# Optimization experiments

Measured on AMD Instinct MI355X. Metric: run time of the kernel, lower is better.

Reference implementation:

```python
import jax, jax.numpy as jnp
import numpy as np

DIM = 512
HEADS = 8
HEAD_DIM = DIM // HEADS
SCALING = float(np.sqrt(HEAD_DIM))
B, S = 8, 2048


def setup_inputs() -> dict:
    key = jax.random.key(0)
    ks = jax.random.split(key, 6)
    x = jax.random.normal(ks[0], (B, S, DIM), dtype=jnp.float32)
    mask = jax.random.randint(ks[1], (B, S), 0, 2).astype(bool)
    mask = mask.at[:, 0].set(False)  # guarantee at least one unmasked key per row
    lim_qkv = 1.0 / np.sqrt(DIM)
    Wqkv = jax.random.uniform(ks[2], (3 * DIM, DIM), minval=-lim_qkv, maxval=lim_qkv, dtype=jnp.float32)
    bqkv = jax.random.uniform(ks[3], (3 * DIM,), minval=-lim_qkv, maxval=lim_qkv, dtype=jnp.float32)
    Wout = jax.random.uniform(ks[4], (DIM, DIM), minval=-lim_qkv, maxval=lim_qkv, dtype=jnp.float32)
    bout = jax.random.uniform(ks[5], (DIM,), minval=-lim_qkv, maxval=lim_qkv, dtype=jnp.float32)
    ln_g = jnp.ones((DIM,), dtype=jnp.float32)
    ln_b = jnp.zeros((DIM,), dtype=jnp.float32)
    return {"x": x, "mask": mask, "Wqkv": Wqkv, "bqkv": bqkv, "Wout": Wout, "bout": bout, "ln_g": ln_g, "ln_b": ln_b}


def reference(x, mask, Wqkv, bqkv, Wout, bout, ln_g, ln_b):
    b, s, _ = x.shape
    qkv = x @ Wqkv.T + bqkv                                   # [b, s, 3*dim]
    qkv = qkv.reshape(b, s, HEADS, HEAD_DIM, 3)               # torch reshape semantics (interleaved)
    q = qkv[..., 0]                                           # [b, s, h, d]
    k = qkv[..., 1]
    v = jax.nn.elu(qkv[..., 2])
    attn = jnp.einsum('bqhd,bkhd->bhqk', q, k) / SCALING      # [b, h, s, s]
    bias = jnp.where(mask[:, None, None, :], -jnp.inf, 0.0).astype(attn.dtype)
    attn = jax.nn.softmax(attn + bias, axis=-1)
    out = jnp.einsum('bhqk,bkhd->bqhd', attn, v).reshape(b, s, DIM)
    out = out @ Wout.T + bout
    mu = jnp.mean(out, axis=-1, keepdims=True)
    var = jnp.var(out, axis=-1, keepdims=True)
    out = (out - mu) / jnp.sqrt(var + 1e-5) * ln_g + ln_b
    return jax.nn.elu(out)
```

## Files before the change

### kernel.cpp

```cpp
#include <hip/hip_runtime.h>

#define DIM 512
#define HEADS 8
#define HD 64
#define NB 8
#define NS 2048
#define SCALE_INV 0.125f
#define NEG_BIG -1e30f
#define QSZ 8388608

typedef __attribute__((ext_vector_type(8))) short bf16x8;
typedef __attribute__((ext_vector_type(4))) float f32x4;

__device__ __forceinline__ float elu_f(float x) {
    return x > 0.0f ? x : (__expf(x) - 1.0f);
}
__device__ __forceinline__ short f2bf(float x) {
    union { float f; unsigned u; } v; v.f = x;
    unsigned r = v.u + 0x7FFFu + ((v.u >> 16) & 1u);
    return (short)(r >> 16);
}
__device__ __forceinline__ unsigned pack_bf_t(float a, float b) {
    union { float f; unsigned u; } va, vb; va.f = a; vb.f = b;
    return (va.u >> 16) | (vb.u & 0xFFFF0000u);
}

#define X4 2097152
#define W14 196608
#define W24 65536
__global__ __launch_bounds__(256) void prep(
    const float* __restrict__ x, const float* __restrict__ Wqkv,
    const float* __restrict__ bqkv, const float* __restrict__ Wout,
    short* __restrict__ xb, short* __restrict__ Wp,
    float* __restrict__ bp, short* __restrict__ Wob)
{
    int i = blockIdx.x * 256 + threadIdx.x;
    if (i < X4) {
        float4 v = *(const float4*)(x + (size_t)i * 4);
        ushort4 o; o.x = (unsigned short)f2bf(v.x); o.y = (unsigned short)f2bf(v.y);
        o.z = (unsigned short)f2bf(v.z); o.w = (unsigned short)f2bf(v.w);
        *(ushort4*)(xb + (size_t)i * 4) = o;
    } else if (i < X4 + W14) {
        int j = i - X4;
        int np = j >> 7, k = (j & 127) * 4;
        int w = np >> 9, h = (np >> 6) & 7, d = np & 63;
        int n = h * 192 + d * 3 + w;
        float4 v = *(const float4*)(Wqkv + (size_t)n * 512 + k);
        ushort4 o; o.x = (unsigned short)f2bf(v.x); o.y = (unsigned short)f2bf(v.y);
        o.z = (unsigned short)f2bf(v.z); o.w = (unsigned short)f2bf(v.w);
        *(ushort4*)(Wp + (size_t)np * 512 + k) = o;
    } else if (i < X4 + W14 + W24) {
        int j = i - X4 - W14;
        float4 v = *(const float4*)(Wout + (size_t)j * 4);
        ushort4 o; o.x = (unsigned short)f2bf(v.x); o.y = (unsigned short)f2bf(v.y);
        o.z = (unsigned short)f2bf(v.z); o.w = (unsigned short)f2bf(v.w);
        *(ushort4*)(Wob + (size_t)j * 4) = o;
    } else {
        int j = i - X4 - W14 - W24;
        int w = j >> 9, h = (j >> 6) & 7, d = j & 63;
        bp[j] = bqkv[h * 192 + d * 3 + w];
    }
}

__global__ __launch_bounds__(256) void qkv_mfma(
    const short* __restrict__ A, const short* __restrict__ Bw,
    const float* __restrict__ bp, short* __restrict__ QKV)
{
    __shared__ short smem[2 * 128 * 64];
    short* As = smem;
    short* Bs = smem + 128 * 64;
    const int t = threadIdx.x, lane = t & 63, wv = t >> 6;
    const int c = lane & 15, quad = lane >> 4;
    const int wr = wv >> 1, wc = wv & 1;
    const int m0 = blockIdx.x * 128, n0 = blockIdx.y * 128;
    f32x4 acc[4][4];
    #pragma unroll
    for (int mi = 0; mi < 4; ++mi)
        #pragma unroll
        for (int nj = 0; nj < 4; ++nj)
            #pragma unroll
            for (int i = 0; i < 4; ++i) acc[mi][nj][i] = 0.0f;

    for (int k0 = 0; k0 < 512; k0 += 64) {
        if (k0) __syncthreads();
        #pragma unroll
        for (int p = 0; p < 4; ++p) {
            int idx = p * 256 + t, r = idx >> 3, cb = idx & 7;
            *(uint4*)&As[r * 64 + ((cb ^ (r & 7)) * 8)] =
                *(const uint4*)(A + (size_t)(m0 + r) * 512 + k0 + cb * 8);
            *(uint4*)&Bs[r * 64 + ((cb ^ (r & 7)) * 8)] =
                *(const uint4*)(Bw + (size_t)(n0 + r) * 512 + k0 + cb * 8);
        }
        __syncthreads();
        bf16x8 af[4][2], bfr[4][2];
        #pragma unroll
        for (int mi = 0; mi < 4; ++mi) {
            int ar = wr * 64 + mi * 16 + c;
            af[mi][0] = *(const bf16x8*)&As[ar * 64 + ((quad       ^ (ar & 7)) * 8)];
            af[mi][1] = *(const bf16x8*)&As[ar * 64 + (((4 + quad) ^ (ar & 7)) * 8)];
        }
        #pragma unroll
        for (int nj = 0; nj < 4; ++nj) {
            int br = wc * 64 + nj * 16 + c;
            bfr[nj][0] = *(const bf16x8*)&Bs[br * 64 + ((quad       ^ (br & 7)) * 8)];
            bfr[nj][1] = *(const bf16x8*)&Bs[br * 64 + (((4 + quad) ^ (br & 7)) * 8)];
        }
        #pragma unroll
        for (int mi = 0; mi < 4; ++mi)
            #pragma unroll
            for (int nj = 0; nj < 4; ++nj) {
                acc[mi][nj] = __builtin_amdgcn_mfma_f32_16x16x32_bf16(af[mi][0], bfr[nj][0], acc[mi][nj], 0, 0, 0);
                acc[mi][nj] = __builtin_amdgcn_mfma_f32_16x16x32_bf16(af[mi][1], bfr[nj][1], acc[mi][nj], 0, 0, 0);
            }
    }

    const int w  = n0 >> 9;
    const int b  = m0 >> 11;
    const int hh = ((n0 + wc * 64) >> 6) & 7;
    float bv[4];
    #pragma unroll
    for (int nj = 0; nj < 4; ++nj) bv[nj] = bp[n0 + wc * 64 + nj * 16 + c];

    if (w < 2) {
        short* out = QKV + (size_t)w * QSZ + (size_t)(b * 8 + hh) * NS * 64;
        #pragma unroll
        for (int mi = 0; mi < 4; ++mi)
            #pragma unroll
            for (int i = 0; i < 4; ++i) {
                int s = (m0 & (NS - 1)) + wr * 64 + mi * 16 + quad * 4 + i;
                #pragma unroll
                for (int nj = 0; nj < 4; ++nj)
                    out[(size_t)s * 64 + nj * 16 + c] = f2bf(acc[mi][nj][i] + bv[nj]);
            }
    } else {
        __syncthreads();
        short* T = smem;
        #pragma unroll
        for (int mi = 0; mi < 4; ++mi)
            #pragma unroll
            for (int i = 0; i < 4; ++i) {
                int ml = wr * 64 + mi * 16 + quad * 4 + i;
                int mb = ml >> 3, mr = ml & 7;
                #pragma unroll
                for (int nj = 0; nj < 4; ++nj) {
                    int nl = wc * 64 + nj * 16 + c;
                    T[nl * 128 + ((mb ^ (nl & 15)) * 8) + mr] =
                        f2bf(elu_f(acc[mi][nj][i] + bv[nj]));
                }
            }
        __syncthreads();
        short* Vt = QKV + (size_t)2 * QSZ;
        #pragma unroll
        for (int p = 0; p < 8; ++p) {
            int idx = p * 256 + t, row = idx >> 4, ch = idx & 15;
            uint4 v = *(const uint4*)&T[row * 128 + ((ch ^ (row & 15)) * 8)];
            int d = row & 63;
            int h2 = ((n0 + row) >> 6) & 7;
            int sg = (m0 & (NS - 1)) + ch * 8;
            int kt = sg >> 6, ks = sg & 63;
            *(uint4*)(Vt + (((size_t)(b * 8 + h2) * 32 + kt) * 64 + d) * 64 + ks) = v;
        }
    }
}

__global__ __launch_bounds__(256, 4) void attn_mfma(
    const short* __restrict__ Qg, const short* __restrict__ Kg,
    const short* __restrict__ Vg, const int* __restrict__ mask,
    short* __restrict__ O)
{
    __shared__ short QP[64 * 64];
    __shared__ short Ks[64 * 64];
    __shared__ short Vs[64 * 64];
    __shared__ float msk[64];

    const int t = threadIdx.x;
    const int lane = t & 63;
    const int wv = t >> 6;
    const int c = lane & 15;
    const int quad = lane >> 4;
    const int bid = blockIdx.x;
    const int qt = bid & 31;
    const int h  = (bid >> 5) & 7;
    const int b  = bid >> 8;
    const int g  = b * 8 + h;
    const size_t base = (size_t)g * NS * HD;
    const int q0 = qt * 64;

    #pragma unroll
    for (int p = 0; p < 2; ++p) {
        int idx = p * 256 + t, r = idx >> 3, cb = idx & 7;
        *(uint4*)&QP[r * 64 + ((cb ^ (r & 7)) * 8)] =
            *(const uint4*)(Qg + base + (size_t)(q0 + r) * HD + cb * 8);
    }
    __syncthreads();

    const int mq = wv * 16 + c;
    const bf16x8 bq0 = *(const bf16x8*)&QP[mq * 64 + ((quad       ^ (mq & 7)) * 8)];
    const bf16x8 bq1 = *(const bf16x8*)&QP[mq * 64 + (((4 + quad) ^ (mq & 7)) * 8)];

    f32x4 o[4];
    #pragma unroll
    for (int dc = 0; dc < 4; ++dc)
        #pragma unroll
        for (int i = 0; i < 4; ++i) o[dc][i] = 0.0f;
    float lp = 0.0f;

    const int prow = wv * 16 + c;
    const int prot = 8 * (c & 7);

    for (int kt = 0; kt < 32; ++kt) {
        const int k0 = kt * 64;
        __syncthreads();
        #pragma unroll
        for (int p = 0; p < 2; ++p) {
            int idx = p * 256 + t, r = idx >> 3, cb = idx & 7;
            *(uint4*)&Ks[r * 64 + ((cb ^ (r & 7)) * 8)] =
                *(const uint4*)(Kg + base + (size_t)(k0 + r) * HD + cb * 8);
            *(uint4*)&Vs[r * 64 + (((cb * 8 + 8 * (r & 7)) & 63))] =
                *(const uint4*)(Vg + (((size_t)g * 32 + kt) * 64 + r) * 64 + cb * 8);
        }
        if (t < 64) msk[t] = mask[b * NS + k0 + t] ? NEG_BIG : 0.0f;
        __syncthreads();

        f32x4 st[4];
        #pragma unroll
        for (int ks = 0; ks < 4; ++ks) {
            int kr = ks * 16 + c;
            bf16x8 ak0 = *(const bf16x8*)&Ks[kr * 64 + ((quad       ^ (kr & 7)) * 8)];
            bf16x8 ak1 = *(const bf16x8*)&Ks[kr * 64 + (((4 + quad) ^ (kr & 7)) * 8)];
            f32x4 a = {0.0f, 0.0f, 0.0f, 0.0f};
            a = __builtin_amdgcn_mfma_f32_16x16x32_bf16(ak0, bq0, a, 0, 0, 0);
            a = __builtin_amdgcn_mfma_f32_16x16x32_bf16(ak1, bq1, a, 0, 0, 0);
            st[ks] = a;
        }

        #pragma unroll
        for (int ks = 0; ks < 4; ++ks) {
            float4 mb = *(const float4*)&msk[ks * 16 + quad * 4];
            float p0 = __expf(st[ks][0] * SCALE_INV + mb.x);
            float p1 = __expf(st[ks][1] * SCALE_INV + mb.y);
            float p2 = __expf(st[ks][2] * SCALE_INV + mb.z);
            float p3 = __expf(st[ks][3] * SCALE_INV + mb.w);
            lp += (p0 + p1) + (p2 + p3);
            uint2 pk;
            pk.x = pack_bf_t(p0, p1);
            pk.y = pack_bf_t(p2, p3);
            *(uint2*)&QP[prow * 64 + ((ks * 16 + quad * 4 + prot) & 63)] = pk;
        }

        bf16x8 bp0 = *(const bf16x8*)&QP[prow * 64 + ((quad * 8 + prot) & 63)];
        bf16x8 bp1 = *(const bf16x8*)&QP[prow * 64 + ((32 + quad * 8 + prot) & 63)];
        #pragma unroll
        for (int dc = 0; dc < 4; ++dc) {
            int d = dc * 16 + c;
            int vrot = 8 * (d & 7);
            bf16x8 av0 = *(const bf16x8*)&Vs[d * 64 + ((quad * 8 + vrot) & 63)];
            bf16x8 av1 = *(const bf16x8*)&Vs[d * 64 + ((32 + quad * 8 + vrot) & 63)];
            o[dc] = __builtin_amdgcn_mfma_f32_16x16x32_bf16(av0, bp0, o[dc], 0, 0, 0);
            o[dc] = __builtin_amdgcn_mfma_f32_16x16x32_bf16(av1, bp1, o[dc], 0, 0, 0);
        }
    }

    lp += __shfl_xor(lp, 16);
    lp += __shfl_xor(lp, 32);
    float inv = 1.0f / lp;

    int q = q0 + wv * 16 + c;
    short* orow = O + ((size_t)(b * NS + q)) * DIM + h * HD + quad * 4;
    #pragma unroll
    for (int dc = 0; dc < 4; ++dc) {
        uint2 pk;
        pk.x = (unsigned)(unsigned short)f2bf(o[dc][0] * inv)
             | ((unsigned)(unsigned short)f2bf(o[dc][1] * inv) << 16);
        pk.y = (unsigned)(unsigned short)f2bf(o[dc][2] * inv)
             | ((unsigned)(unsigned short)f2bf(o[dc][3] * inv) << 16);
        *(uint2*)(orow + dc * 16) = pk;
    }
}

__global__ __launch_bounds__(256) void out_mfma(
    const short* __restrict__ A, const short* __restrict__ Bw,
    const float* __restrict__ bias, float* __restrict__ Z)
{
    __shared__ short smem[2 * 128 * 64];
    short* As = smem;
    short* Bs = smem + 128 * 64;
    const int t = threadIdx.x, lane = t & 63, wv = t >> 6;
    const int c = lane & 15, quad = lane >> 4;
    const int wr = wv >> 1, wc = wv & 1;
    const int m0 = blockIdx.x * 128, n0 = blockIdx.y * 128;
    f32x4 acc[4][4];
    #pragma unroll
    for (int mi = 0; mi < 4; ++mi)
        #pragma unroll
        for (int nj = 0; nj < 4; ++nj)
            #pragma unroll
            for (int i = 0; i < 4; ++i) acc[mi][nj][i] = 0.0f;

    for (int k0 = 0; k0 < 512; k0 += 64) {
        if (k0) __syncthreads();
        #pragma unroll
        for (int p = 0; p < 4; ++p) {
            int idx = p * 256 + t, r = idx >> 3, cb = idx & 7;
            *(uint4*)&As[r * 64 + ((cb ^ (r & 7)) * 8)] =
                *(const uint4*)(A + (size_t)(m0 + r) * 512 + k0 + cb * 8);
            *(uint4*)&Bs[r * 64 + ((cb ^ (r & 7)) * 8)] =
                *(const uint4*)(Bw + (size_t)(n0 + r) * 512 + k0 + cb * 8);
        }
        __syncthreads();
        bf16x8 af[4][2], bfr[4][2];
        #pragma unroll
        for (int mi = 0; mi < 4; ++mi) {
            int ar = wr * 64 + mi * 16 + c;
            af[mi][0] = *(const bf16x8*)&As[ar * 64 + ((quad       ^ (ar & 7)) * 8)];
            af[mi][1] = *(const bf16x8*)&As[ar * 64 + (((4 + quad) ^ (ar & 7)) * 8)];
        }
        #pragma unroll
        for (int nj = 0; nj < 4; ++nj) {
            int br = wc * 64 + nj * 16 + c;
            bfr[nj][0] = *(const bf16x8*)&Bs[br * 64 + ((quad       ^ (br & 7)) * 8)];
            bfr[nj][1] = *(const bf16x8*)&Bs[br * 64 + (((4 + quad) ^ (br & 7)) * 8)];
        }
        #pragma unroll
        for (int mi = 0; mi < 4; ++mi)
            #pragma unroll
            for (int nj = 0; nj < 4; ++nj) {
                acc[mi][nj] = __builtin_amdgcn_mfma_f32_16x16x32_bf16(af[mi][0], bfr[nj][0], acc[mi][nj], 0, 0, 0);
                acc[mi][nj] = __builtin_amdgcn_mfma_f32_16x16x32_bf16(af[mi][1], bfr[nj][1], acc[mi][nj], 0, 0, 0);
            }
    }
    #pragma unroll
    for (int mi = 0; mi < 4; ++mi)
        #pragma unroll
        for (int i = 0; i < 4; ++i) {
            int mrow = m0 + wr * 64 + mi * 16 + quad * 4 + i;
            #pragma unroll
            for (int nj = 0; nj < 4; ++nj) {
                int n = n0 + wc * 64 + nj * 16 + c;
                Z[(size_t)mrow * 512 + n] = acc[mi][nj][i] + bias[n];
            }
        }
}

__global__ __launch_bounds__(256) void ln_elu(
    const float* __restrict__ Z, const float* __restrict__ g,
    const float* __restrict__ bt, float* __restrict__ out)
{
    const int row = blockIdx.x;
    const float* z = Z + (size_t)row * DIM;
    const int t = threadIdx.x;
    float v0 = z[t], v1 = z[t + 256];
    float s  = v0 + v1;
    float ss = v0 * v0 + v1 * v1;
    #pragma unroll
    for (int off = 32; off > 0; off >>= 1) {
        s  += __shfl_down(s, off);
        ss += __shfl_down(ss, off);
    }
    __shared__ float rs[4], rss[4];
    int wid = t >> 6, lane = t & 63;
    if (lane == 0) { rs[wid] = s; rss[wid] = ss; }
    __syncthreads();
    float S1 = rs[0] + rs[1] + rs[2] + rs[3];
    float S2 = rss[0] + rss[1] + rss[2] + rss[3];
    float mu  = S1 * (1.0f / DIM);
    float var = S2 * (1.0f / DIM) - mu * mu;
    float rstd = rsqrtf(var + 1e-5f);
    float y0 = (v0 - mu) * rstd * g[t]       + bt[t];
    float y1 = (v1 - mu) * rstd * g[t + 256] + bt[t + 256];
    out[(size_t)row * DIM + t]       = elu_f(y0);
    out[(size_t)row * DIM + t + 256] = elu_f(y1);
}

extern "C" void kernel_launch(void* const* d_in, const int* in_sizes, int n_in,
                              void* d_out, int out_size, void* d_ws, size_t ws_size,
                              hipStream_t stream)
{
    const float* x    = (const float*)d_in[0];
    const int*   mask = (const int*)d_in[1];
    const float* Wqkv = (const float*)d_in[2];
    const float* bqkv = (const float*)d_in[3];
    const float* Wout = (const float*)d_in[4];
    const float* bout = (const float*)d_in[5];
    const float* ln_g = (const float*)d_in[6];
    const float* ln_b = (const float*)d_in[7];
    float* out = (float*)d_out;

    short* xb   = (short*)d_ws;
    short* Wp   = xb + QSZ;
    short* Wob  = Wp + 786432;
    short* QKV  = Wob + 262144;
    short* ATTb = QKV + 3 * (size_t)QSZ;
    float* bp   = (float*)(ATTb + QSZ);
    float* Zb   = bp + 1536;

    prep<<<9222, 256, 0, stream>>>(x, Wqkv, bqkv, Wout, xb, Wp, bp, Wob);
    qkv_mfma<<<dim3(128, 12), 256, 0, stream>>>(xb, Wp, bp, QKV);
    attn_mfma<<<2048, 256, 0, stream>>>(QKV, QKV + QSZ, QKV + 2 * (size_t)QSZ, mask, ATTb);
    out_mfma<<<dim3(128, 4), 256, 0, stream>>>(ATTb, Wob, bout, Zb);
    ln_elu<<<NB * NS, 256, 0, stream>>>(Zb, ln_g, ln_b, out);
}
```

Before: 271.5 us.

## Double-buffer attention K/V via direct global-to-LDS loads with 128-query blocks

Attention now uses 512-thread blocks covering 128 queries. K, V and mask tiles are double-buffered in shared memory and loaded with global_load_lds, so the next tile's fetch overlaps compute and one barrier per iteration is removed. The QKV and output GEMMs also switch to direct-to-LDS loads, and all three matrix-core loops raise wave priority with s_setprio. The mask-to-float conversion moves into the prep kernel. The cost is more shared memory per block and reliance on the compiler placing the correct waitcnt before each barrier. The mask buffer is also placed in the tail of the Z scratch buffer.

```diff
diff --git a/kernel.cpp b/kernel.cpp
--- a/kernel.cpp
+++ b/kernel.cpp
@@ -25,14 +25,27 @@
     return (va.u >> 16) | (vb.u & 0xFFFF0000u);
 }
 
+__device__ __forceinline__ void gload16(const void* g, void* l) {
+    __builtin_amdgcn_global_load_lds(
+        (const __attribute__((address_space(1))) unsigned*)g,
+        (__attribute__((address_space(3))) unsigned*)l, 16, 0, 0);
+}
+__device__ __forceinline__ void gload4(const void* g, void* l) {
+    __builtin_amdgcn_global_load_lds(
+        (const __attribute__((address_space(1))) unsigned*)g,
+        (__attribute__((address_space(3))) unsigned*)l, 4, 0, 0);
+}
+
 #define X4 2097152
 #define W14 196608
 #define W24 65536
 __global__ __launch_bounds__(256) void prep(
     const float* __restrict__ x, const float* __restrict__ Wqkv,
     const float* __restrict__ bqkv, const float* __restrict__ Wout,
+    const int* __restrict__ mask,
     short* __restrict__ xb, short* __restrict__ Wp,
-    float* __restrict__ bp, short* __restrict__ Wob)
+    float* __restrict__ bp, short* __restrict__ Wob,
+    float* __restrict__ maskf)
 {
     int i = blockIdx.x * 256 + threadIdx.x;
     if (i < X4) {
@@ -55,10 +68,13 @@
         ushort4 o; o.x = (unsigned short)f2bf(v.x); o.y = (unsigned short)f2bf(v.y);
         o.z = (unsigned short)f2bf(v.z); o.w = (unsigned short)f2bf(v.w);
         *(ushort4*)(Wob + (size_t)j * 4) = o;
-    } else {
+    } else if (i < X4 + W14 + W24 + 1536) {
         int j = i - X4 - W14 - W24;
         int w = j >> 9, h = (j >> 6) & 7, d = j & 63;
         bp[j] = bqkv[h * 192 + d * 3 + w];
+    } else {
+        int j = i - X4 - W14 - W24 - 1536;
+        maskf[j] = mask[j] ? NEG_BIG : 0.0f;
     }
 }
 
@@ -72,6 +88,8 @@
     const int t = threadIdx.x, lane = t & 63, wv = t >> 6;
     const int c = lane & 15, quad = lane >> 4;
     const int wr = wv >> 1, wc = wv & 1;
+    const int rsub = lane >> 3;
+    const int csA = (lane & 7) ^ rsub;
     const int m0 = blockIdx.x * 128, n0 = blockIdx.y * 128;
     f32x4 acc[4][4];
     #pragma unroll
@@ -85,11 +103,9 @@
         if (k0) __syncthreads();
         #pragma unroll
         for (int p = 0; p < 4; ++p) {
-            int idx = p * 256 + t, r = idx >> 3, cb = idx & 7;
-            *(uint4*)&As[r * 64 + ((cb ^ (r & 7)) * 8)] =
-                *(const uint4*)(A + (size_t)(m0 + r) * 512 + k0 + cb * 8);
-            *(uint4*)&Bs[r * 64 + ((cb ^ (r & 7)) * 8)] =
-                *(const uint4*)(Bw + (size_t)(n0 + r) * 512 + k0 + cb * 8);
+            int r = p * 32 + wv * 8 + rsub;
+            gload16(A  + (size_t)(m0 + r) * 512 + k0 + csA * 8, &As[(p * 4 + wv) * 512]);
+            gload16(Bw + (size_t)(n0 + r) * 512 + k0 + csA * 8, &Bs[(p * 4 + wv) * 512]);
         }
         __syncthreads();
         bf16x8 af[4][2], bfr[4][2];
@@ -105,6 +121,7 @@
             bfr[nj][0] = *(const bf16x8*)&Bs[br * 64 + ((quad       ^ (br & 7)) * 8)];
             bfr[nj][1] = *(const bf16x8*)&Bs[br * 64 + (((4 + quad) ^ (br & 7)) * 8)];
         }
+        __builtin_amdgcn_s_setprio(1);
         #pragma unroll
         for (int mi = 0; mi < 4; ++mi)
             #pragma unroll
@@ -112,6 +129,7 @@
                 acc[mi][nj] = __builtin_amdgcn_mfma_f32_16x16x32_bf16(af[mi][0], bfr[nj][0], acc[mi][nj], 0, 0, 0);
                 acc[mi][nj] = __builtin_amdgcn_mfma_f32_16x16x32_bf16(af[mi][1], bfr[nj][1], acc[mi][nj], 0, 0, 0);
             }
+        __builtin_amdgcn_s_setprio(0);
     }
 
     const int w  = n0 >> 9;
@@ -163,15 +181,15 @@
     }
 }
 
-__global__ __launch_bounds__(256, 4) void attn_mfma(
+__global__ __launch_bounds__(512, 6) void attn_mfma(
     const short* __restrict__ Qg, const short* __restrict__ Kg,
-    const short* __restrict__ Vg, const int* __restrict__ mask,
+    const short* __restrict__ Vg, const float* __restrict__ maskf,
     short* __restrict__ O)
 {
-    __shared__ short QP[64 * 64];
-    __shared__ short Ks[64 * 64];
-    __shared__ short Vs[64 * 64];
-    __shared__ float msk[64];
+    __shared__ short QP[128 * 64];
+    __shared__ short Ks[2][64 * 64];
+    __shared__ short Vs[2][64 * 64];
+    __shared__ float msk[2][64];
 
     const int t = threadIdx.x;
     const int lane = t & 63;
@@ -179,18 +197,27 @@
     const int c = lane & 15;
     const int quad = lane >> 4;
     const int bid = blockIdx.x;
-    const int qt = bid & 31;
-    const int h  = (bid >> 5) & 7;
-    const int b  = bid >> 8;
+    const int qt = bid & 15;
+    const int h  = (bid >> 4) & 7;
+    const int b  = bid >> 7;
     const int g  = b * 8 + h;
     const size_t base = (size_t)g * NS * HD;
-    const int q0 = qt * 64;
+    const int q0 = qt * 128;
+
+    const int rsub = lane >> 3;
+    const int csA  = (lane & 7) ^ rsub;
+    const int csV  = ((lane & 7) - rsub) & 7;
 
     #pragma unroll
     for (int p = 0; p < 2; ++p) {
-        int idx = p * 256 + t, r = idx >> 3, cb = idx & 7;
-        *(uint4*)&QP[r * 64 + ((cb ^ (r & 7)) * 8)] =
-            *(const uint4*)(Qg + base + (size_t)(q0 + r) * HD + cb * 8);
+        int r = wv * 16 + p * 8 + rsub;
+        gload16(Qg + base + (size_t)(q0 + r) * HD + csA * 8, &QP[(wv * 2 + p) * 512]);
+    }
+    {
+        int r = wv * 8 + rsub;
+        gload16(Kg + base + (size_t)r * HD + csA * 8, &Ks[0][wv * 512]);
+        gload16(Vg + (((size_t)g * 32 + 0) * 64 + r) * 64 + csV * 8, &Vs[0][wv * 512]);
+        if (wv == 0) gload4(maskf + (size_t)b * NS + lane, &msk[0][0]);
     }
     __syncthreads();
 
@@ -198,6 +225,13 @@
     const bf16x8 bq0 = *(const bf16x8*)&QP[mq * 64 + ((quad       ^ (mq & 7)) * 8)];
     const bf16x8 bq1 = *(const bf16x8*)&QP[mq * 64 + (((4 + quad) ^ (mq & 7)) * 8)];
 
+    {
+        int r = wv * 8 + rsub;
+        gload16(Kg + base + (size_t)(64 + r) * HD + csA * 8, &Ks[1][wv * 512]);
+        gload16(Vg + (((size_t)g * 32 + 1) * 64 + r) * 64 + csV * 8, &Vs[1][wv * 512]);
+        if (wv == 0) gload4(maskf + (size_t)b * NS + 64 + lane, &msk[1][0]);
+    }
+
     f32x4 o[4];
     #pragma unroll
     for (int dc = 0; dc < 4; ++dc)
@@ -209,34 +243,27 @@
     const int prot = 8 * (c & 7);
 
     for (int kt = 0; kt < 32; ++kt) {
-        const int k0 = kt * 64;
-        __syncthreads();
-        #pragma unroll
-        for (int p = 0; p < 2; ++p) {
-            int idx = p * 256 + t, r = idx >> 3, cb = idx & 7;
-            *(uint4*)&Ks[r * 64 + ((cb ^ (r & 7)) * 8)] =
-                *(const uint4*)(Kg + base + (size_t)(k0 + r) * HD + cb * 8);
-            *(uint4*)&Vs[r * 64 + (((cb * 8 + 8 * (r & 7)) & 63))] =
-                *(const uint4*)(Vg + (((size_t)g * 32 + kt) * 64 + r) * 64 + cb * 8);
-        }
-        if (t < 64) msk[t] = mask[b * NS + k0 + t] ? NEG_BIG : 0.0f;
-        __syncthreads();
+        const int cur = kt & 1;
+        const short* Kc = Ks[cur];
+        const short* Vc = Vs[cur];
 
         f32x4 st[4];
+        __builtin_amdgcn_s_setprio(1);
         #pragma unroll
         for (int ks = 0; ks < 4; ++ks) {
             int kr = ks * 16 + c;
-            bf16x8 ak0 = *(const bf16x8*)&Ks[kr * 64 + ((quad       ^ (kr & 7)) * 8)];
-            bf16x8 ak1 = *(const bf16x8*)&Ks[kr * 64 + (((4 + quad) ^ (kr & 7)) * 8)];
+            bf16x8 ak0 = *(const bf16x8*)&Kc[kr * 64 + ((quad       ^ (kr & 7)) * 8)];
+            bf16x8 ak1 = *(const bf16x8*)&Kc[kr * 64 + (((4 + quad) ^ (kr & 7)) * 8)];
             f32x4 a = {0.0f, 0.0f, 0.0f, 0.0f};
             a = __builtin_amdgcn_mfma_f32_16x16x32_bf16(ak0, bq0, a, 0, 0, 0);
             a = __builtin_amdgcn_mfma_f32_16x16x32_bf16(ak1, bq1, a, 0, 0, 0);
             st[ks] = a;
         }
+        __builtin_amdgcn_s_setprio(0);
 
         #pragma unroll
         for (int ks = 0; ks < 4; ++ks) {
-            float4 mb = *(const float4*)&msk[ks * 16 + quad * 4];
+            float4 mb = *(const float4*)&msk[cur][ks * 16 + quad * 4];
             float p0 = __expf(st[ks][0] * SCALE_INV + mb.x);
             float p1 = __expf(st[ks][1] * SCALE_INV + mb.y);
             float p2 = __expf(st[ks][2] * SCALE_INV + mb.z);
@@ -250,14 +277,26 @@
 
         bf16x8 bp0 = *(const bf16x8*)&QP[prow * 64 + ((quad * 8 + prot) & 63)];
         bf16x8 bp1 = *(const bf16x8*)&QP[prow * 64 + ((32 + quad * 8 + prot) & 63)];
+        __builtin_amdgcn_s_setprio(1);
         #pragma unroll
         for (int dc = 0; dc < 4; ++dc) {
             int d = dc * 16 + c;
             int vrot = 8 * (d & 7);
-            bf16x8 av0 = *(const bf16x8*)&Vs[d * 64 + ((quad * 8 + vrot) & 63)];
-            bf16x8 av1 = *(const bf16x8*)&Vs[d * 64 + ((32 + quad * 8 + vrot) & 63)];
+            bf16x8 av0 = *(const bf16x8*)&Vc[d * 64 + ((quad * 8 + vrot) & 63)];
+            bf16x8 av1 = *(const bf16x8*)&Vc[d * 64 + ((32 + quad * 8 + vrot) & 63)];
             o[dc] = __builtin_amdgcn_mfma_f32_16x16x32_bf16(av0, bp0, o[dc], 0, 0, 0);
             o[dc] = __builtin_amdgcn_mfma_f32_16x16x32_bf16(av1, bp1, o[dc], 0, 0, 0);
+        }
+        __builtin_amdgcn_s_setprio(0);
+
+        __syncthreads();
+
+        if (kt + 2 < 32) {
+            int r = wv * 8 + rsub;
+            int k0n = (kt + 2) * 64;
+            gload16(Kg + base + (size_t)(k0n + r) * HD + csA * 8, &Ks[cur][wv * 512]);
+            gload16(Vg + (((size_t)g * 32 + (kt + 2)) * 64 + r) * 64 + csV * 8, &Vs[cur][wv * 512]);
+            if (wv == 0) gload4(maskf + (size_t)b * NS + k0n + lane, &msk[cur][0]);
         }
     }
 
@@ -288,6 +327,8 @@
     const int t = threadIdx.x, lane = t & 63, wv = t >> 6;
     const int c = lane & 15, quad = lane >> 4;
     const int wr = wv >> 1, wc = wv & 1;
+    const int rsub = lane >> 3;
+    const int csA = (lane & 7) ^ rsub;
     const int m0 = blockIdx.x * 128, n0 = blockIdx.y * 128;
     f32x4 acc[4][4];
     #pragma unroll
@@ -301,11 +342,9 @@
         if (k0) __syncthreads();
         #pragma unroll
         for (int p = 0; p < 4; ++p) {
-            int idx = p * 256 + t, r = idx >> 3, cb = idx & 7;
-            *(uint4*)&As[r * 64 + ((cb ^ (r & 7)) * 8)] =
-                *(const uint4*)(A + (size_t)(m0 + r) * 512 + k0 + cb * 8);
-            *(uint4*)&Bs[r * 64 + ((cb ^ (r & 7)) * 8)] =
-                *(const uint4*)(Bw + (size_t)(n0 + r) * 512 + k0 + cb * 8);
+            int r = p * 32 + wv * 8 + rsub;
+            gload16(A  + (size_t)(m0 + r) * 512 + k0 + csA * 8, &As[(p * 4 + wv) * 512]);
+            gload16(Bw + (size_t)(n0 + r) * 512 + k0 + csA * 8, &Bs[(p * 4 + wv) * 512]);
         }
         __syncthreads();
         bf16x8 af[4][2], bfr[4][2];
@@ -321,6 +360,7 @@
             bfr[nj][0] = *(const bf16x8*)&Bs[br * 64 + ((quad       ^ (br & 7)) * 8)];
             bfr[nj][1] = *(const bf16x8*)&Bs[br * 64 + (((4 + quad) ^ (br & 7)) * 8)];
         }
+        __builtin_amdgcn_s_setprio(1);
         #pragma unroll
         for (int mi = 0; mi < 4; ++mi)
             #pragma unroll
@@ -328,6 +368,7 @@
                 acc[mi][nj] = __builtin_amdgcn_mfma_f32_16x16x32_bf16(af[mi][0], bfr[nj][0], acc[mi][nj], 0, 0, 0);
                 acc[mi][nj] = __builtin_amdgcn_mfma_f32_16x16x32_bf16(af[mi][1], bfr[nj][1], acc[mi][nj], 0, 0, 0);
             }
+        __builtin_amdgcn_s_setprio(0);
     }
     #pragma unroll
     for (int mi = 0; mi < 4; ++mi)
@@ -393,10 +434,11 @@
     short* ATTb = QKV + 3 * (size_t)QSZ;
     float* bp   = (float*)(ATTb + QSZ);
     float* Zb   = bp + 1536;
-
-    prep<<<9222, 256, 0, stream>>>(x, Wqkv, bqkv, Wout, xb, Wp, bp, Wob);
+    float* maskf = Zb + (size_t)QSZ - 16384;
+
+    prep<<<9286, 256, 0, stream>>>(x, Wqkv, bqkv, Wout, mask, xb, Wp, bp, Wob, maskf);
     qkv_mfma<<<dim3(128, 12), 256, 0, stream>>>(xb, Wp, bp, QKV);
-    attn_mfma<<<2048, 256, 0, stream>>>(QKV, QKV + QSZ, QKV + 2 * (size_t)QSZ, mask, ATTb);
+    attn_mfma<<<1024, 512, 0, stream>>>(QKV, QKV + QSZ, QKV + 2 * (size_t)QSZ, maskf, ATTb);
     out_mfma<<<dim3(128, 4), 256, 0, stream>>>(ATTb, Wob, bout, Zb);
     ln_elu<<<NB * NS, 256, 0, stream>>>(Zb, ln_g, ln_b, out);
 }
```

New measurement: 253.4 us. 1.07x faster.
